# Performance work log

Measured on AMD Instinct MI355X. Metric: run time of the kernel, lower is better.

Reference implementation:

```python
import jax, jax.numpy as jnp
import numpy as np

N_HEAD, D_HEAD, D_MODEL, MAX_LEN = 16, 64, 1024, 64
T, B = 1024, 4
SCALE = 1.0 / D_HEAD ** 0.5


def setup_inputs() -> dict:
    key = jax.random.key(0)
    k1, k2, k3, k4 = jax.random.split(key, 4)
    s = 0.02
    w = jax.random.normal(k1, (T, B, D_MODEL), jnp.float32)
    Wqkv = jax.random.normal(k2, (3 * N_HEAD * D_HEAD, D_MODEL), jnp.float32) * s
    pos_emb = jax.random.normal(k3, (2 * MAX_LEN + 1, D_HEAD), jnp.float32) * s
    Wo = jax.random.normal(k4, (D_MODEL, N_HEAD * D_HEAD), jnp.float32) * s
    i = jnp.arange(T)
    # causal mask, 3D path of the original: [qlen, klen, bsz], True = masked
    attn_mask = jnp.broadcast_to((i[None, :] > i[:, None])[:, :, None], (T, T, B))
    return {"w": w, "attn_mask": attn_mask, "Wqkv": Wqkv, "pos_emb": pos_emb, "Wo": Wo}


def reference(w, attn_mask, Wqkv, pos_emb, Wo):
    qlen, bsz, _ = w.shape
    klen = qlen
    # qkv projection (no bias), chunk into q, k, v
    heads = jnp.einsum('tbd,ed->tbe', w, Wqkv)            # [T, B, 3*H*Dh]
    q, k, v = jnp.split(heads, 3, axis=-1)
    q = q.reshape(qlen, bsz, N_HEAD, D_HEAD).transpose(1, 2, 0, 3) * SCALE  # [B,H,T,Dh]
    k = k.reshape(klen, bsz, N_HEAD, D_HEAD).transpose(1, 2, 0, 3)
    v = v.reshape(klen, bsz, N_HEAD, D_HEAD).transpose(1, 2, 0, 3)
    # learnable relative position embeddings r[q_pos, k_pos, Dh]
    i = jnp.arange(klen)
    rel = jnp.clip(i[None, :] - i[:, None], -MAX_LEN, MAX_LEN) + MAX_LEN   # [T, T]
    r = pos_emb[rel]                                                       # [T, T, Dh]
    # content score + relative-position score (q already scaled)
    qk = jnp.einsum('bhqd,bhkd->bhqk', q, k)
    qr = jnp.einsum('bhqd,qkd->bhqk', q, r)
    score = qk + qr                                                        # [B,H,T,T]
    m = attn_mask.transpose(2, 0, 1)[:, None]                              # [B,1,T,T]
    score = jnp.where(m, -jnp.inf, score)
    attn = jax.nn.softmax(score, axis=-1)                                  # coverage
    # content context + position context
    ctx = jnp.einsum('bhqk,bhkd->bhqd', attn, v) + jnp.einsum('bhqk,qkd->bhqd', attn, r)
    attn_vec = ctx.transpose(0, 2, 1, 3).reshape(bsz, qlen, N_HEAD * D_HEAD)
    out = jnp.einsum('bte,de->btd', attn_vec, Wo)                          # [B,T,D]
    return jnp.swapaxes(out, 0, 1)                                         # [T,B,D]
```

## Files before the change

kernel.cpp:

```cpp
#include <hip/hip_runtime.h>
#include <hip/hip_bf16.h>
#include <math.h>

#define N_HEAD 16
#define D_HEAD 64
#define T_SEQ 1024
#define BATCH 4
#define QSCALE 0.180336879f

typedef float f32x4 __attribute__((ext_vector_type(4)));
typedef short bf16x8 __attribute__((ext_vector_type(8)));
typedef short bf16x4v __attribute__((ext_vector_type(4)));

#define AS1(p) ((const __attribute__((address_space(1))) void*)(p))
#define AS3(p) ((__attribute__((address_space(3))) void*)(p))

__device__ inline bf16x8 ld8(const __hip_bfloat16* p) {
    bf16x4v lo = *(const bf16x4v*)p;
    bf16x4v hi = *(const bf16x4v*)(p + 4);
    return __builtin_shufflevector(lo, hi, 0, 1, 2, 3, 4, 5, 6, 7);
}

__global__ __launch_bounds__(256) void cast_all(
    const float* __restrict__ s0, __hip_bfloat16* __restrict__ d0, int n0,
    const float* __restrict__ s1, __hip_bfloat16* __restrict__ d1, int n1,
    const float* __restrict__ s2, __hip_bfloat16* __restrict__ d2, int n2) {
    int i = (blockIdx.x * 256 + threadIdx.x) * 8;
    const float* src;
    __hip_bfloat16* dst;
    if (i < n0) { src = s0 + i; dst = d0 + i; }
    else if ((i -= n0) < n1) { src = s1 + i; dst = d1 + i; }
    else if ((i -= n1) < n2) { src = s2 + i; dst = d2 + i; }
    else return;
    float4 a = *(const float4*)src;
    float4 b = *(const float4*)(src + 4);
    __hip_bfloat16 t[8];
    t[0] = __float2bfloat16(a.x); t[1] = __float2bfloat16(a.y);
    t[2] = __float2bfloat16(a.z); t[3] = __float2bfloat16(a.w);
    t[4] = __float2bfloat16(b.x); t[5] = __float2bfloat16(b.y);
    t[6] = __float2bfloat16(b.z); t[7] = __float2bfloat16(b.w);
    *(uint4*)dst = *(const uint4*)t;
}

__global__ __launch_bounds__(256) void qkv_gemm_mfma(
    const __hip_bfloat16* __restrict__ A,
    const __hip_bfloat16* __restrict__ B,
    const float* __restrict__ P,
    __hip_bfloat16* __restrict__ Qb, __hip_bfloat16* __restrict__ Kb,
    __hip_bfloat16* __restrict__ Vtb) {
    constexpr int Kd = 1024;
    __shared__ __hip_bfloat16 As[128 * 32];
    __shared__ __hip_bfloat16 Bs[128 * 32];
    const int tid = threadIdx.x;
    const int w = tid >> 6, lane = tid & 63;
    const int lanelo = lane & 15, quad = lane >> 4;
    const int wm = (w >> 1) * 64, wn = (w & 1) * 64;
    const int m0 = blockIdx.y * 128, n0 = blockIdx.x * 128;

    const __hip_bfloat16* Ag = A + (size_t)(m0 + w * 16 + (lane >> 2)) * Kd + (lane & 3) * 8;
    const __hip_bfloat16* Bg = B + (size_t)(n0 + w * 16 + (lane >> 2)) * Kd + (lane & 3) * 8;
    __hip_bfloat16* AsW0 = As + w * 16 * 32;
    __hip_bfloat16* AsW1 = As + (64 + w * 16) * 32;
    __hip_bfloat16* BsW0 = Bs + w * 16 * 32;
    __hip_bfloat16* BsW1 = Bs + (64 + w * 16) * 32;

    f32x4 acc[4][4];
#pragma unroll
    for (int i = 0; i < 4; i++)
#pragma unroll
        for (int j = 0; j < 4; j++) acc[i][j] = (f32x4){0.f, 0.f, 0.f, 0.f};

    for (int k0 = 0; k0 < Kd; k0 += 32) {
        __syncthreads();
        __builtin_amdgcn_global_load_lds(AS1(Ag + k0), AS3(AsW0), 16, 0, 0);
        __builtin_amdgcn_global_load_lds(AS1(Ag + 64 * Kd + k0), AS3(AsW1), 16, 0, 0);
        __builtin_amdgcn_global_load_lds(AS1(Bg + k0), AS3(BsW0), 16, 0, 0);
        __builtin_amdgcn_global_load_lds(AS1(Bg + 64 * Kd + k0), AS3(BsW1), 16, 0, 0);
        __syncthreads();
        bf16x8 af[4], bfr[4];
#pragma unroll
        for (int i = 0; i < 4; i++)
            af[i] = *(const bf16x8*)(As + (wm + i * 16 + lanelo) * 32 + quad * 8);
#pragma unroll
        for (int j = 0; j < 4; j++)
            bfr[j] = *(const bf16x8*)(Bs + (wn + j * 16 + lanelo) * 32 + quad * 8);
#pragma unroll
        for (int i = 0; i < 4; i++)
#pragma unroll
            for (int j = 0; j < 4; j++)
                acc[i][j] = __builtin_amdgcn_mfma_f32_16x16x32_bf16(af[i], bfr[j], acc[i][j], 0, 0, 0);
    }

    const int part = n0 >> 10;
    float p0v[4] = {0.f, 0.f, 0.f, 0.f};
    if (part == 2) {
#pragma unroll
        for (int j = 0; j < 4; j++) p0v[j] = P[j * 16 + lanelo];
    }
#pragma unroll
    for (int i = 0; i < 4; i++)
#pragma unroll
        for (int j = 0; j < 4; j++)
#pragma unroll
            for (int reg = 0; reg < 4; reg++) {
                const int row = m0 + wm + i * 16 + quad * 4 + reg;
                const int col = n0 + wn + j * 16 + lanelo;
                const int t = row >> 2, b = row & 3;
                const int e = col & 1023, h = e >> 6, d = e & 63;
                const float v = acc[i][j][reg];
                if (part == 0)
                    Qb[((size_t)(b * 16 + h) * 1024 + t) * 64 + d] = __float2bfloat16(v * QSCALE);
                else if (part == 1)
                    Kb[((size_t)(b * 16 + h) * 1024 + t) * 64 + d] = __float2bfloat16(v);
                else
                    Vtb[((size_t)(b * 16 + h) * 64 + d) * 1024 + t] = __float2bfloat16(v + p0v[j]);
            }
}

__global__ __launch_bounds__(256) void out_gemm_mfma(
    const __hip_bfloat16* __restrict__ A,
    const __hip_bfloat16* __restrict__ B,
    float* __restrict__ out) {
    constexpr int Kd = 1024;
    __shared__ __hip_bfloat16 As[128 * 32];
    __shared__ __hip_bfloat16 Bs[64 * 32];
    const int tid = threadIdx.x;
    const int w = tid >> 6, lane = tid & 63;
    const int lanelo = lane & 15, quad = lane >> 4;
    const int wm = (w >> 1) * 64, wn = (w & 1) * 32;
    const int m0 = blockIdx.y * 128, n0 = blockIdx.x * 64;

    const __hip_bfloat16* Ag = A + (size_t)(m0 + w * 16 + (lane >> 2)) * Kd + (lane & 3) * 8;
    const __hip_bfloat16* Bg = B + (size_t)(n0 + w * 16 + (lane >> 2)) * Kd + (lane & 3) * 8;
    __hip_bfloat16* AsW0 = As + w * 16 * 32;
    __hip_bfloat16* AsW1 = As + (64 + w * 16) * 32;
    __hip_bfloat16* BsW0 = Bs + w * 16 * 32;

    f32x4 acc[4][2];
#pragma unroll
    for (int i = 0; i < 4; i++)
#pragma unroll
        for (int j = 0; j < 2; j++) acc[i][j] = (f32x4){0.f, 0.f, 0.f, 0.f};

    for (int k0 = 0; k0 < Kd; k0 += 32) {
        __syncthreads();
        __builtin_amdgcn_global_load_lds(AS1(Ag + k0), AS3(AsW0), 16, 0, 0);
        __builtin_amdgcn_global_load_lds(AS1(Ag + 64 * Kd + k0), AS3(AsW1), 16, 0, 0);
        __builtin_amdgcn_global_load_lds(AS1(Bg + k0), AS3(BsW0), 16, 0, 0);
        __syncthreads();
        bf16x8 af[4], bfr[2];
#pragma unroll
        for (int i = 0; i < 4; i++)
            af[i] = *(const bf16x8*)(As + (wm + i * 16 + lanelo) * 32 + quad * 8);
#pragma unroll
        for (int j = 0; j < 2; j++)
            bfr[j] = *(const bf16x8*)(Bs + (wn + j * 16 + lanelo) * 32 + quad * 8);
#pragma unroll
        for (int i = 0; i < 4; i++)
#pragma unroll
            for (int j = 0; j < 2; j++)
                acc[i][j] = __builtin_amdgcn_mfma_f32_16x16x32_bf16(af[i], bfr[j], acc[i][j], 0, 0, 0);
    }

#pragma unroll
    for (int i = 0; i < 4; i++)
#pragma unroll
        for (int j = 0; j < 2; j++)
#pragma unroll
            for (int reg = 0; reg < 4; reg++) {
                const int row = m0 + wm + i * 16 + quad * 4 + reg;
                const int col = n0 + wn + j * 16 + lanelo;
                const int b = row >> 10, t = row & 1023;
                out[(size_t)(t * 4 + b) * 1024 + col] = acc[i][j][reg];
            }
}

__global__ __launch_bounds__(256) void flash_attn(
    const __hip_bfloat16* __restrict__ Qb,
    const __hip_bfloat16* __restrict__ Kb,
    const __hip_bfloat16* __restrict__ Vtb,
    const float* __restrict__ P,
    __hip_bfloat16* __restrict__ av) {
    __shared__ __hip_bfloat16 Ks[64][72];
    __shared__ __hip_bfloat16 Vs[64][72];
    __shared__ __hip_bfloat16 Pl[4][16][68];
    __shared__ __hip_bfloat16 Pband[4][2][16][68];
    __shared__ __hip_bfloat16 QPl[4][2][16][66];

    const int px = blockIdx.x;
    const int TB = 15 - px, TS = px;
    const int bh = blockIdx.y;
    const int b = bh >> 4, h = bh & 15;
    const int tid = threadIdx.x;
    const int w = tid >> 6, lane = tid & 63;
    const int lanelo = lane & 15, quad = lane >> 4;
    const size_t qkbase = (size_t)bh * 1024 * 64;
    const size_t vbase  = (size_t)bh * 64 * 1024;

    const int sr = tid >> 2;
    const int sc = (tid & 3) << 4;
    const __hip_bfloat16* kgb = Kb + qkbase + (size_t)sr * 64 + sc;
    const __hip_bfloat16* vgb = Vtb + vbase + (size_t)sr * 1024 + sc;

    {
        short* pb = (short*)&Pband[w][0][0][0];
        for (int i = lane; i < 2 * 16 * 68; i += 64) pb[i] = 0;
    }

    bf16x8 aqb0, aqb1, aqs0, aqs1;
    {
        const __hip_bfloat16* qrb = Qb + qkbase + (size_t)(TB * 64 + w * 16 + lanelo) * 64;
        aqb0 = *(const bf16x8*)(qrb + quad * 8);
        aqb1 = *(const bf16x8*)(qrb + 32 + quad * 8);
        const __hip_bfloat16* qrs = Qb + qkbase + (size_t)(TS * 64 + w * 16 + lanelo) * 64;
        aqs0 = *(const bf16x8*)(qrs + quad * 8);
        aqs1 = *(const bf16x8*)(qrs + 32 + quad * 8);
    }

#pragma unroll
    for (int jj = 0; jj < 5; jj++) {
        const float* prow = P + (size_t)(jj * 16 + lanelo) * 64 + quad * 8;
        float4 pa = *(const float4*)prow;
        float4 pb = *(const float4*)(prow + 4);
        float4 pc = *(const float4*)(prow + 32);
        float4 pd = *(const float4*)(prow + 36);
        __hip_bfloat16 t0[8], t1[8];
        t0[0] = __float2bfloat16(pa.x); t0[1] = __float2bfloat16(pa.y);
        t0[2] = __float2bfloat16(pa.z); t0[3] = __float2bfloat16(pa.w);
        t0[4] = __float2bfloat16(pb.x); t0[5] = __float2bfloat16(pb.y);
        t0[6] = __float2bfloat16(pb.z); t0[7] = __float2bfloat16(pb.w);
        t1[0] = __float2bfloat16(pc.x); t1[1] = __float2bfloat16(pc.y);
        t1[2] = __float2bfloat16(pc.z); t1[3] = __float2bfloat16(pc.w);
        t1[4] = __float2bfloat16(pd.x); t1[5] = __float2bfloat16(pd.y);
        t1[6] = __float2bfloat16(pd.z); t1[7] = __float2bfloat16(pd.w);
        f32x4 accB = (f32x4){0.f, 0.f, 0.f, 0.f};
        accB = __builtin_amdgcn_mfma_f32_16x16x32_bf16(aqb0, *(const bf16x8*)t0, accB, 0, 0, 0);
        accB = __builtin_amdgcn_mfma_f32_16x16x32_bf16(aqb1, *(const bf16x8*)t1, accB, 0, 0, 0);
        f32x4 accS = (f32x4){0.f, 0.f, 0.f, 0.f};
        accS = __builtin_amdgcn_mfma_f32_16x16x32_bf16(aqs0, *(const bf16x8*)t0, accS, 0, 0, 0);
        accS = __builtin_amdgcn_mfma_f32_16x16x32_bf16(aqs1, *(const bf16x8*)t1, accS, 0, 0, 0);
#pragma unroll
        for (int reg = 0; reg < 4; reg++) {
            QPl[w][0][quad * 4 + reg][jj * 16 + lanelo] = __float2bfloat16(accB[reg]);
            QPl[w][1][quad * 4 + reg][jj * 16 + lanelo] = __float2bfloat16(accS[reg]);
        }
    }
    float qp0b[4], qp0s[4];
#pragma unroll
    for (int reg = 0; reg < 4; reg++) {
        qp0b[reg] = (float)QPl[w][0][quad * 4 + reg][0];
        qp0s[reg] = (float)QPl[w][1][quad * 4 + reg][0];
    }

    f32x4 o_accB[4], o_lB, o_accS[4], o_lS;
#pragma unroll
    for (int dt = 0; dt < 4; dt++) {
        o_accB[dt] = (f32x4){0.f, 0.f, 0.f, 0.f};
        o_accS[dt] = (f32x4){0.f, 0.f, 0.f, 0.f};
    }
    o_lB = (f32x4){0.f, 0.f, 0.f, 0.f};
    o_lS = (f32x4){0.f, 0.f, 0.f, 0.f};
    const short one_bf = 0x3F80;
    const bf16x8 vones = {one_bf, one_bf, one_bf, one_bf, one_bf, one_bf, one_bf, one_bf};

    auto do_qtile = [&](int tq, int Tq, const bf16x8& a0, const bf16x8& a1,
                        const float* qp0, f32x4* o_acc, f32x4& o_l, int kt) {
        f32x4 s_acc[4];
#pragma unroll
        for (int ct = 0; ct < 4; ct++) {
            bf16x8 b0 = *(const bf16x8*)&Ks[ct * 16 + lanelo][quad * 8];
            bf16x8 b1 = *(const bf16x8*)&Ks[ct * 16 + lanelo][32 + quad * 8];
            f32x4 acc = (f32x4){0.f, 0.f, 0.f, 0.f};
            acc = __builtin_amdgcn_mfma_f32_16x16x32_bf16(a0, b0, acc, 0, 0, 0);
            acc = __builtin_amdgcn_mfma_f32_16x16x32_bf16(a1, b1, acc, 0, 0, 0);
            s_acc[ct] = acc;
        }
        const int q0 = Tq * 64 + w * 16;
        const int obase = q0 - kt * 64;
        if (kt < Tq - 1) {
#pragma unroll
            for (int ct = 0; ct < 4; ct++)
#pragma unroll
                for (int reg = 0; reg < 4; reg++) {
                    const float p = __builtin_exp2f(s_acc[ct][reg] + qp0[reg]);
                    Pl[w][quad * 4 + reg][ct * 16 + lanelo] = __float2bfloat16(p);
                }
        } else {
#pragma unroll
            for (int ct = 0; ct < 4; ct++)
#pragma unroll
                for (int reg = 0; reg < 4; reg++) {
                    const int rloc = quad * 4 + reg;
                    const int kl = ct * 16 + lanelo;
                    const int o = obase + rloc - kl;
                    const int idx = (o >= 64 || o < 0) ? 0 : (64 - o);
                    const float add = (float)QPl[w][tq][rloc][idx];
                    const float p = (o < 0) ? 0.f : __builtin_exp2f(s_acc[ct][reg] + add);
                    const __hip_bfloat16 pbv = __float2bfloat16(p);
                    Pl[w][rloc][kl] = pbv;
                    if (o >= 0 && o <= 63) Pband[w][tq][rloc][63 - o] = pbv;
                }
        }
#pragma unroll
        for (int c = 0; c < 2; c++) {
            bf16x8 ap = ld8(&Pl[w][lanelo][c * 32 + quad * 8]);
#pragma unroll
            for (int dt = 0; dt < 4; dt++) {
                bf16x8 bv = *(const bf16x8*)&Vs[dt * 16 + lanelo][c * 32 + quad * 8];
                o_acc[dt] = __builtin_amdgcn_mfma_f32_16x16x32_bf16(ap, bv, o_acc[dt], 0, 0, 0);
            }
            o_l = __builtin_amdgcn_mfma_f32_16x16x32_bf16(ap, vones, o_l, 0, 0, 0);
        }
    };

    uint4 rk0, rk1, rv0, rv1;
    rk0 = *(const uint4*)(kgb);
    rk1 = *(const uint4*)(kgb + 8);
    rv0 = *(const uint4*)(vgb);
    rv1 = *(const uint4*)(vgb + 8);

    for (int kt = 0; kt <= TB; kt++) {
        __syncthreads();
        *(uint4*)&Ks[sr][sc]     = rk0;
        *(uint4*)&Ks[sr][sc + 8] = rk1;
        *(uint4*)&Vs[sr][sc]     = rv0;
        *(uint4*)&Vs[sr][sc + 8] = rv1;
        if (kt < TB) {
            const __hip_bfloat16* kg = kgb + (size_t)(kt + 1) * 4096;
            const __hip_bfloat16* vg = vgb + (size_t)(kt + 1) * 64;
            rk0 = *(const uint4*)(kg);
            rk1 = *(const uint4*)(kg + 8);
            rv0 = *(const uint4*)(vg);
            rv1 = *(const uint4*)(vg + 8);
        }
        __syncthreads();

        do_qtile(0, TB, aqb0, aqb1, qp0b, o_accB, o_lB, kt);
        if (kt <= TS) do_qtile(1, TS, aqs0, aqs1, qp0s, o_accS, o_lS, kt);
    }

#pragma unroll
    for (int tq = 0; tq < 2; tq++) {
        f32x4* o_acc = tq == 0 ? o_accB : o_accS;
        f32x4& o_l   = tq == 0 ? o_lB : o_lS;
        const int q0 = (tq == 0 ? TB : TS) * 64 + w * 16;
#pragma unroll
        for (int c = 0; c < 2; c++) {
            bf16x8 ab = ld8(&Pband[w][tq][lanelo][c * 32 + quad * 8]);
#pragma unroll
            for (int dt = 0; dt < 4; dt++) {
                const int d = dt * 16 + lanelo;
                const float p0 = P[d];
                __hip_bfloat16 tb[8];
#pragma unroll
                for (int jj = 0; jj < 8; jj++) {
                    const int kk = c * 32 + quad * 8 + jj;
                    tb[jj] = __float2bfloat16(P[(kk + 1) * 64 + d] - p0);
                }
                o_acc[dt] = __builtin_amdgcn_mfma_f32_16x16x32_bf16(ab, *(const bf16x8*)tb, o_acc[dt], 0, 0, 0);
            }
        }
        float rinv[4];
#pragma unroll
        for (int reg = 0; reg < 4; reg++) rinv[reg] = 1.0f / o_l[reg];
#pragma unroll
        for (int dt = 0; dt < 4; dt++) {
            const int cdim = dt * 16 + lanelo;
#pragma unroll
            for (int reg = 0; reg < 4; reg++) {
                const int q = q0 + quad * 4 + reg;
                av[((size_t)(b * 1024 + q)) * 1024 + h * 64 + cdim] =
                    __float2bfloat16(o_acc[dt][reg] * rinv[reg]);
            }
        }
    }
}

extern "C" void kernel_launch(void* const* d_in, const int* in_sizes, int n_in,
                              void* d_out, int out_size, void* d_ws, size_t ws_size,
                              hipStream_t stream) {
    const float* w       = (const float*)d_in[0];
    const float* Wqkv    = (const float*)d_in[2];
    const float* pos_emb = (const float*)d_in[3];
    const float* Wo      = (const float*)d_in[4];
    float* out = (float*)d_out;

    const size_t SZ = (size_t)BATCH * N_HEAD * T_SEQ * D_HEAD;
    __hip_bfloat16* wb     = (__hip_bfloat16*)d_ws;
    __hip_bfloat16* Wqkvb  = wb + SZ;
    __hip_bfloat16* Wob    = Wqkvb + 3 * 1024 * 1024;
    __hip_bfloat16* Qb     = Wob + 1024 * 1024;
    __hip_bfloat16* Kb     = Qb + SZ;
    __hip_bfloat16* Vtb    = Kb + SZ;
    __hip_bfloat16* AVb    = Vtb + SZ;

    const int n_w = 4096 * 1024, n_wqkv = 3072 * 1024, n_wo = 1024 * 1024;
    const int n_tot = n_w + n_wqkv + n_wo;
    cast_all<<<n_tot / 2048, 256, 0, stream>>>(w, wb, n_w, Wqkv, Wqkvb, n_wqkv, Wo, Wob, n_wo);

    qkv_gemm_mfma<<<dim3(3072 / 128, 4096 / 128), 256, 0, stream>>>(wb, Wqkvb, pos_emb, Qb, Kb, Vtb);
    flash_attn<<<dim3(8, 64), 256, 0, stream>>>(Qb, Kb, Vtb, pos_emb, AVb);
    out_gemm_mfma<<<dim3(1024 / 64, 4096 / 128), 256, 0, stream>>>(AVb, Wob, out);
}
```

Baseline: 190.1 us.

## Rewrite QKV GEMM as 256x256 tile with 4-stage LDS pipeline

Replaces the 128x128 QKV projection GEMM with a 512-thread 256x256 tile kernel. It uses a four-buffer LDS ring prefetched ahead of use, XOR-swizzled LDS columns to avoid bank conflicts, and s_setprio around the MFMA bursts. The aim is to hide global load latency, raise arithmetic intensity per tile and cut LDS conflicts. In exchange it needs 128 KB of dynamic LDS, leaves only 192 blocks and adds more barriers, so occupancy and wave balance on the device could suffer.

```diff
diff --git a/kernel.cpp b/kernel.cpp
--- a/kernel.cpp
+++ b/kernel.cpp
@@ -42,79 +42,135 @@
     *(uint4*)dst = *(const uint4*)t;
 }
 
-__global__ __launch_bounds__(256) void qkv_gemm_mfma(
+__global__ __launch_bounds__(512, 2) void qkv_gemm_256(
     const __hip_bfloat16* __restrict__ A,
     const __hip_bfloat16* __restrict__ B,
     const float* __restrict__ P,
     __hip_bfloat16* __restrict__ Qb, __hip_bfloat16* __restrict__ Kb,
     __hip_bfloat16* __restrict__ Vtb) {
-    constexpr int Kd = 1024;
-    __shared__ __hip_bfloat16 As[128 * 32];
-    __shared__ __hip_bfloat16 Bs[128 * 32];
+    extern __shared__ __align__(16) __hip_bfloat16 lds[];
+    __hip_bfloat16* Asl = lds;
+    __hip_bfloat16* Bsl = lds + 4 * 8192;
+
     const int tid = threadIdx.x;
     const int w = tid >> 6, lane = tid & 63;
     const int lanelo = lane & 15, quad = lane >> 4;
-    const int wm = (w >> 1) * 64, wn = (w & 1) * 64;
-    const int m0 = blockIdx.y * 128, n0 = blockIdx.x * 128;
-
-    const __hip_bfloat16* Ag = A + (size_t)(m0 + w * 16 + (lane >> 2)) * Kd + (lane & 3) * 8;
-    const __hip_bfloat16* Bg = B + (size_t)(n0 + w * 16 + (lane >> 2)) * Kd + (lane & 3) * 8;
-    __hip_bfloat16* AsW0 = As + w * 16 * 32;
-    __hip_bfloat16* AsW1 = As + (64 + w * 16) * 32;
-    __hip_bfloat16* BsW0 = Bs + w * 16 * 32;
-    __hip_bfloat16* BsW1 = Bs + (64 + w * 16) * 32;
-
-    f32x4 acc[4][4];
-#pragma unroll
-    for (int i = 0; i < 4; i++)
+    const int wr = w >> 2, wc = w & 3;
+    const int m0 = blockIdx.y * 256, n0 = blockIdx.x * 256;
+
+    const int srow = lane >> 2;
+    const int scol = ((lane & 3) ^ ((lane >> 2) & 3)) * 8;
+    const __hip_bfloat16* Ag0 = A + (size_t)(m0 + w * 16 + srow) * 1024 + scol;
+    const __hip_bfloat16* Ag1 = Ag0 + (size_t)128 * 1024;
+    const __hip_bfloat16* Bg0 = B + (size_t)(n0 + w * 16 + srow) * 1024 + scol;
+    const __hip_bfloat16* Bg1 = Bg0 + (size_t)128 * 1024;
+
+    auto STAGE = [&](const __hip_bfloat16* g0, const __hip_bfloat16* g1,
+                     __hip_bfloat16* s, int koff) {
+        __builtin_amdgcn_global_load_lds(AS1(g0 + koff), AS3(s + w * 512), 16, 0, 0);
+        __builtin_amdgcn_global_load_lds(AS1(g1 + koff), AS3(s + 4096 + w * 512), 16, 0, 0);
+    };
+
+    const int cbs = (quad * 8) ^ ((lanelo & 3) * 8);
+    auto LD4 = [&](const __hip_bfloat16* s, int rbase, bf16x8* f) {
+#pragma unroll
+        for (int m = 0; m < 4; m++)
+            f[m] = *(const bf16x8*)(s + (size_t)(rbase + m * 16) * 32 + cbs);
+    };
+
+    f32x4 acc[8][4];
+#pragma unroll
+    for (int i = 0; i < 8; i++)
 #pragma unroll
         for (int j = 0; j < 4; j++) acc[i][j] = (f32x4){0.f, 0.f, 0.f, 0.f};
 
-    for (int k0 = 0; k0 < Kd; k0 += 32) {
-        __syncthreads();
-        __builtin_amdgcn_global_load_lds(AS1(Ag + k0), AS3(AsW0), 16, 0, 0);
-        __builtin_amdgcn_global_load_lds(AS1(Ag + 64 * Kd + k0), AS3(AsW1), 16, 0, 0);
-        __builtin_amdgcn_global_load_lds(AS1(Bg + k0), AS3(BsW0), 16, 0, 0);
-        __builtin_amdgcn_global_load_lds(AS1(Bg + 64 * Kd + k0), AS3(BsW1), 16, 0, 0);
-        __syncthreads();
-        bf16x8 af[4], bfr[4];
-#pragma unroll
-        for (int i = 0; i < 4; i++)
-            af[i] = *(const bf16x8*)(As + (wm + i * 16 + lanelo) * 32 + quad * 8);
-#pragma unroll
-        for (int j = 0; j < 4; j++)
-            bfr[j] = *(const bf16x8*)(Bs + (wn + j * 16 + lanelo) * 32 + quad * 8);
-#pragma unroll
-        for (int i = 0; i < 4; i++)
-#pragma unroll
-            for (int j = 0; j < 4; j++)
-                acc[i][j] = __builtin_amdgcn_mfma_f32_16x16x32_bf16(af[i], bfr[j], acc[i][j], 0, 0, 0);
-    }
+#define MFMA16(CH)                                                                 \
+    do {                                                                           \
+        __builtin_amdgcn_s_setprio(1);                                             \
+        _Pragma("unroll") for (int m_ = 0; m_ < 4; m_++)                           \
+            _Pragma("unroll") for (int n_ = 0; n_ < 4; n_++)                       \
+                acc[(CH) * 4 + m_][n_] = __builtin_amdgcn_mfma_f32_16x16x32_bf16(  \
+                    a[m_], b[n_], acc[(CH) * 4 + m_][n_], 0, 0, 0);                \
+        __builtin_amdgcn_s_setprio(0);                                             \
+    } while (0)
+
+    STAGE(Ag0, Ag1, Asl + 0 * 8192, 0);
+    STAGE(Bg0, Bg1, Bsl + 0 * 8192, 0);
+    STAGE(Ag0, Ag1, Asl + 1 * 8192, 32);
+    STAGE(Bg0, Bg1, Bsl + 1 * 8192, 32);
+    STAGE(Ag0, Ag1, Asl + 2 * 8192, 64);
+    STAGE(Bg0, Bg1, Bsl + 2 * 8192, 64);
+    asm volatile("s_waitcnt vmcnt(8)" ::: "memory");
+    __builtin_amdgcn_s_barrier();
+
+    const int ra = wr * 128 + lanelo;
+    const int rb = wc * 64 + lanelo;
+
+    for (int t = 0; t < 16; ++t) {
+        bf16x8 a[4], b[4];
+        const __hip_bfloat16* As0 = Asl + ((2 * t) & 3) * 8192;
+        const __hip_bfloat16* Bs0 = Bsl + ((2 * t) & 3) * 8192;
+        const __hip_bfloat16* As1 = Asl + ((2 * t + 1) & 3) * 8192;
+        const __hip_bfloat16* Bs1 = Bsl + ((2 * t + 1) & 3) * 8192;
+        const int t1 = t + 1 < 16 ? t + 1 : 15;
+        const int t2 = t + 2 < 16 ? t + 2 : 15;
+
+        LD4(As0, ra, a);
+        LD4(Bs0, rb, b);
+        STAGE(Ag0, Ag1, Asl + ((2 * t1 + 1) & 3) * 8192, t1 * 64 + 32);
+        __builtin_amdgcn_s_barrier();
+        MFMA16(0);
+        __builtin_amdgcn_s_barrier();
+
+        LD4(As0, ra + 64, a);
+        STAGE(Bg0, Bg1, Bsl + ((2 * t1 + 1) & 3) * 8192, t1 * 64 + 32);
+        __builtin_amdgcn_s_barrier();
+        MFMA16(1);
+        asm volatile("s_waitcnt vmcnt(8)" ::: "memory");
+        __builtin_amdgcn_s_barrier();
+
+        LD4(As1, ra, a);
+        LD4(Bs1, rb, b);
+        STAGE(Ag0, Ag1, Asl + ((2 * t2) & 3) * 8192, t2 * 64);
+        __builtin_amdgcn_s_barrier();
+        MFMA16(0);
+        __builtin_amdgcn_s_barrier();
+
+        LD4(As1, ra + 64, a);
+        STAGE(Bg0, Bg1, Bsl + ((2 * t2) & 3) * 8192, t2 * 64);
+        __builtin_amdgcn_s_barrier();
+        MFMA16(1);
+        asm volatile("s_waitcnt vmcnt(8)" ::: "memory");
+        __builtin_amdgcn_s_barrier();
+    }
+#undef MFMA16
 
     const int part = n0 >> 10;
     float p0v[4] = {0.f, 0.f, 0.f, 0.f};
     if (part == 2) {
 #pragma unroll
-        for (int j = 0; j < 4; j++) p0v[j] = P[j * 16 + lanelo];
-    }
-#pragma unroll
-    for (int i = 0; i < 4; i++)
-#pragma unroll
-        for (int j = 0; j < 4; j++)
-#pragma unroll
-            for (int reg = 0; reg < 4; reg++) {
-                const int row = m0 + wm + i * 16 + quad * 4 + reg;
-                const int col = n0 + wn + j * 16 + lanelo;
-                const int t = row >> 2, b = row & 3;
-                const int e = col & 1023, h = e >> 6, d = e & 63;
-                const float v = acc[i][j][reg];
-                if (part == 0)
-                    Qb[((size_t)(b * 16 + h) * 1024 + t) * 64 + d] = __float2bfloat16(v * QSCALE);
-                else if (part == 1)
-                    Kb[((size_t)(b * 16 + h) * 1024 + t) * 64 + d] = __float2bfloat16(v);
-                else
-                    Vtb[((size_t)(b * 16 + h) * 64 + d) * 1024 + t] = __float2bfloat16(v + p0v[j]);
-            }
+        for (int n = 0; n < 4; n++) p0v[n] = P[n * 16 + lanelo];
+    }
+#pragma unroll
+    for (int ch = 0; ch < 2; ch++)
+#pragma unroll
+        for (int m = 0; m < 4; m++)
+#pragma unroll
+            for (int n = 0; n < 4; n++)
+#pragma unroll
+                for (int reg = 0; reg < 4; reg++) {
+                    const int row = m0 + wr * 128 + ch * 64 + m * 16 + quad * 4 + reg;
+                    const int col = n0 + wc * 64 + n * 16 + lanelo;
+                    const int tt = row >> 2, bb = row & 3;
+                    const int e = col & 1023, h = e >> 6, d = e & 63;
+                    const float v = acc[ch * 4 + m][n][reg];
+                    if (part == 0)
+                        Qb[((size_t)(bb * 16 + h) * 1024 + tt) * 64 + d] = __float2bfloat16(v * QSCALE);
+                    else if (part == 1)
+                        Kb[((size_t)(bb * 16 + h) * 1024 + tt) * 64 + d] = __float2bfloat16(v);
+                    else
+                        Vtb[((size_t)(bb * 16 + h) * 64 + d) * 1024 + tt] = __float2bfloat16(v + p0v[n]);
+                }
 }
 
 __global__ __launch_bounds__(256) void out_gemm_mfma(
@@ -394,11 +450,18 @@
     __hip_bfloat16* Vtb    = Kb + SZ;
     __hip_bfloat16* AVb    = Vtb + SZ;
 
+    static bool qkv_attr_set = false;
+    if (!qkv_attr_set) {
+        hipFuncSetAttribute(reinterpret_cast<const void*>(qkv_gemm_256),
+                            hipFuncAttributeMaxDynamicSharedMemorySize, 131072);
+        qkv_attr_set = true;
+    }
+
     const int n_w = 4096 * 1024, n_wqkv = 3072 * 1024, n_wo = 1024 * 1024;
     const int n_tot = n_w + n_wqkv + n_wo;
     cast_all<<<n_tot / 2048, 256, 0, stream>>>(w, wb, n_w, Wqkv, Wqkvb, n_wqkv, Wo, Wob, n_wo);
 
-    qkv_gemm_mfma<<<dim3(3072 / 128, 4096 / 128), 256, 0, stream>>>(wb, Wqkvb, pos_emb, Qb, Kb, Vtb);
+    qkv_gemm_256<<<dim3(3072 / 256, 4096 / 256), 512, 131072, stream>>>(wb, Wqkvb, pos_emb, Qb, Kb, Vtb);
     flash_attn<<<dim3(8, 64), 256, 0, stream>>>(Qb, Kb, Vtb, pos_emb, AVb);
     out_gemm_mfma<<<dim3(1024 / 64, 4096 / 128), 256, 0, stream>>>(AVb, Wob, out);
 }
```

Result: slower. 211.0 us (+11.0%).

## Remap QKV GEMM blocks per XCD and widen out-GEMM K-tile with swizzle

Applied to the files above, without the earlier changes.

The QKV GEMM now launches a 1D grid and remaps block ids so each of the 8 XCDs works on a contiguous 8x12 tile region, which should improve L2 reuse of the A and B panels. The output GEMM doubles its K step to 64 with larger LDS tiles and an XOR-swizzled layout, halving the number of barrier pairs and avoiding LDS bank conflicts on fragment reads. The costs are more LDS per block in the out GEMM and a grid mapping that is hardcoded to this problem shape and to 8 XCDs.

```diff
diff --git a/kernel.cpp b/kernel.cpp
--- a/kernel.cpp
+++ b/kernel.cpp
@@ -55,7 +55,13 @@
     const int w = tid >> 6, lane = tid & 63;
     const int lanelo = lane & 15, quad = lane >> 4;
     const int wm = (w >> 1) * 64, wn = (w & 1) * 64;
-    const int m0 = blockIdx.y * 128, n0 = blockIdx.x * 128;
+
+    const int bid = blockIdx.x;
+    const int xcd = bid & 7, r = bid >> 3;
+    const int ly = r / 12, lx = r % 12;
+    const int by = (xcd >> 1) * 8 + ly;
+    const int bx = (xcd & 1) * 12 + lx;
+    const int m0 = by * 128, n0 = bx * 128;
 
     const __hip_bfloat16* Ag = A + (size_t)(m0 + w * 16 + (lane >> 2)) * Kd + (lane & 3) * 8;
     const __hip_bfloat16* Bg = B + (size_t)(n0 + w * 16 + (lane >> 2)) * Kd + (lane & 3) * 8;
@@ -122,19 +128,20 @@
     const __hip_bfloat16* __restrict__ B,
     float* __restrict__ out) {
     constexpr int Kd = 1024;
-    __shared__ __hip_bfloat16 As[128 * 32];
-    __shared__ __hip_bfloat16 Bs[64 * 32];
+    __shared__ __hip_bfloat16 As[128 * 64];
+    __shared__ __hip_bfloat16 Bs[64 * 64];
     const int tid = threadIdx.x;
     const int w = tid >> 6, lane = tid & 63;
     const int lanelo = lane & 15, quad = lane >> 4;
     const int wm = (w >> 1) * 64, wn = (w & 1) * 32;
     const int m0 = blockIdx.y * 128, n0 = blockIdx.x * 64;
 
-    const __hip_bfloat16* Ag = A + (size_t)(m0 + w * 16 + (lane >> 2)) * Kd + (lane & 3) * 8;
-    const __hip_bfloat16* Bg = B + (size_t)(n0 + w * 16 + (lane >> 2)) * Kd + (lane & 3) * 8;
-    __hip_bfloat16* AsW0 = As + w * 16 * 32;
-    __hip_bfloat16* AsW1 = As + (64 + w * 16) * 32;
-    __hip_bfloat16* BsW0 = Bs + w * 16 * 32;
+    const int sr = lane >> 3;
+    const int sc = ((lane & 7) ^ sr) * 8;
+    const __hip_bfloat16* Ag = A + (size_t)(m0 + w * 32 + sr) * Kd + sc;
+    const __hip_bfloat16* Bg = B + (size_t)(n0 + w * 16 + sr) * Kd + sc;
+    __hip_bfloat16* AsW = As + w * 2048;
+    __hip_bfloat16* BsW = Bs + w * 1024;
 
     f32x4 acc[4][2];
 #pragma unroll
@@ -142,24 +149,33 @@
 #pragma unroll
         for (int j = 0; j < 2; j++) acc[i][j] = (f32x4){0.f, 0.f, 0.f, 0.f};
 
-    for (int k0 = 0; k0 < Kd; k0 += 32) {
-        __syncthreads();
-        __builtin_amdgcn_global_load_lds(AS1(Ag + k0), AS3(AsW0), 16, 0, 0);
-        __builtin_amdgcn_global_load_lds(AS1(Ag + 64 * Kd + k0), AS3(AsW1), 16, 0, 0);
-        __builtin_amdgcn_global_load_lds(AS1(Bg + k0), AS3(BsW0), 16, 0, 0);
-        __syncthreads();
-        bf16x8 af[4], bfr[2];
+    const int cswz = lanelo & 7;
+
+    for (int k0 = 0; k0 < Kd; k0 += 64) {
+        __syncthreads();
 #pragma unroll
         for (int i = 0; i < 4; i++)
-            af[i] = *(const bf16x8*)(As + (wm + i * 16 + lanelo) * 32 + quad * 8);
-#pragma unroll
-        for (int j = 0; j < 2; j++)
-            bfr[j] = *(const bf16x8*)(Bs + (wn + j * 16 + lanelo) * 32 + quad * 8);
-#pragma unroll
-        for (int i = 0; i < 4; i++)
+            __builtin_amdgcn_global_load_lds(AS1(Ag + k0 + i * 8 * Kd), AS3(AsW + i * 512), 16, 0, 0);
+#pragma unroll
+        for (int i = 0; i < 2; i++)
+            __builtin_amdgcn_global_load_lds(AS1(Bg + k0 + i * 8 * Kd), AS3(BsW + i * 512), 16, 0, 0);
+        __syncthreads();
+#pragma unroll
+        for (int h = 0; h < 2; h++) {
+            const int c16 = (((h * 4 + quad) ^ cswz)) * 8;
+            bf16x8 af[4], bfr[2];
+#pragma unroll
+            for (int i = 0; i < 4; i++)
+                af[i] = *(const bf16x8*)(As + (size_t)(wm + i * 16 + lanelo) * 64 + c16);
 #pragma unroll
             for (int j = 0; j < 2; j++)
-                acc[i][j] = __builtin_amdgcn_mfma_f32_16x16x32_bf16(af[i], bfr[j], acc[i][j], 0, 0, 0);
+                bfr[j] = *(const bf16x8*)(Bs + (size_t)(wn + j * 16 + lanelo) * 64 + c16);
+#pragma unroll
+            for (int i = 0; i < 4; i++)
+#pragma unroll
+                for (int j = 0; j < 2; j++)
+                    acc[i][j] = __builtin_amdgcn_mfma_f32_16x16x32_bf16(af[i], bfr[j], acc[i][j], 0, 0, 0);
+        }
     }
 
 #pragma unroll
@@ -398,7 +414,7 @@
     const int n_tot = n_w + n_wqkv + n_wo;
     cast_all<<<n_tot / 2048, 256, 0, stream>>>(w, wb, n_w, Wqkv, Wqkvb, n_wqkv, Wo, Wob, n_wo);
 
-    qkv_gemm_mfma<<<dim3(3072 / 128, 4096 / 128), 256, 0, stream>>>(wb, Wqkvb, pos_emb, Qb, Kb, Vtb);
+    qkv_gemm_mfma<<<dim3(768), 256, 0, stream>>>(wb, Wqkvb, pos_emb, Qb, Kb, Vtb);
     flash_attn<<<dim3(8, 64), 256, 0, stream>>>(Qb, Kb, Vtb, pos_emb, AVb);
     out_gemm_mfma<<<dim3(1024 / 64, 4096 / 128), 256, 0, stream>>>(AVb, Wob, out);
 }
```

Result: no change. 190.1 us (-0.0%).
